# Performance work log

Measured on AMD Instinct MI355X. Metric: run time of the kernel, lower is better.

Reference implementation:

```python
import jax, jax.numpy as jnp
import numpy as np

NUM_CENTROID = 64
HIDDEN = 768
MAX_SEQ = 128
D = MAX_SEQ * HIDDEN  # 98304 flattened feature dim
NUM_ITERS = 10        # fixed Lloyd iterations (original loops to tol; fixed for jit)


def _cdist(x, c):
    x2 = jnp.sum(x * x, axis=-1, keepdims=True)          # [N,1]
    c2 = jnp.sum(c * c, axis=-1)                          # [K]
    d2 = x2 + c2[None, :] - 2.0 * (x @ c.T)               # [N,K]
    return jnp.sqrt(jnp.maximum(d2, 0.0))


def setup_inputs() -> dict:
    key = jax.random.key(0)
    k1, k2 = jax.random.split(key)
    x = jax.random.normal(k1, (1024, MAX_SEQ, HIDDEN), dtype=jnp.float32)
    # centroid table initialized as Normal(mean=0.07, std=0.39) per the module
    centroid = 0.07 + 0.39 * jax.random.normal(k2, (NUM_CENTROID, D), dtype=jnp.float32)
    return {"x": x, "centroid": centroid}


def reference(x, centroid):
    X = x.reshape(-1, D)                                  # [N, D]
    N = X.shape[0]
    # 'resuming' branch: snap each centroid to its nearest sample
    dis0 = _cdist(X, centroid)                            # [N, K]
    choice_points = jnp.argmin(dis0, axis=0)              # [K]
    state = X[choice_points]                              # [K, D]
    ones = jnp.ones((N,), dtype=X.dtype)

    def step(state, _):
        dis = _cdist(X, state)                            # [N, K]
        choice = jnp.argmin(dis, axis=1)                  # [N]
        sums = jax.ops.segment_sum(X, choice, num_segments=NUM_CENTROID)   # [K, D]
        counts = jax.ops.segment_sum(ones, choice, num_segments=NUM_CENTROID)  # [K]
        nonempty = counts[:, None] > 0
        new_state = jnp.where(nonempty, sums / jnp.maximum(counts[:, None], 1.0), state)
        return new_state, choice

    state, choices = jax.lax.scan(step, state, None, length=NUM_ITERS)
    # returns (new centroids, final cluster assignments) like the module
    return state, choices[-1]
```

## Files before the change

### kernel.cpp

```cpp
#include <hip/hip_runtime.h>
#include <cstddef>
#include <cstdint>


#define N_PTS  1024
#define K_C    64
#define D_DIM  98304
#define ITERS  10
#define SPLITD 64
#define BM     64
#define DC     64
#define LDSP   72
#define NCHK   96
#define CCHK   12
#define GSEG   16
#define NPAIR  36
#define GT     128
#define GDC    32
#define GLP    40

typedef __attribute__((ext_vector_type(8))) short bf16x8;
typedef __attribute__((ext_vector_type(8))) unsigned short ushort8;
typedef __attribute__((ext_vector_type(4))) float f32x4;

__device__ __forceinline__ unsigned short f2bf(float x) {
    unsigned u = __float_as_uint(x);
    u = (u + 0x7FFFu + ((u >> 16) & 1u)) >> 16;
    return (unsigned short)u;
}
__device__ __forceinline__ float bf2f(unsigned short b) {
    return __uint_as_float((unsigned)b << 16);
}
__device__ __forceinline__ void cvt2(float x, unsigned short& h, unsigned short& l) {
    h = f2bf(x);
    l = f2bf(x - bf2f(h));
}

__device__ __forceinline__ float block_sum256(float s) {
    #pragma unroll
    for (int o = 32; o; o >>= 1) s += __shfl_down(s, o);
    __shared__ float red[4];
    int lane = threadIdx.x & 63, w = threadIdx.x >> 6;
    if (lane == 0) red[w] = s;
    __syncthreads();
    return red[0] + red[1] + red[2] + red[3];
}

__global__ __launch_bounds__(256) void convert_kernel(const float* __restrict__ A,
                                                      unsigned short* __restrict__ Ph,
                                                      unsigned short* __restrict__ Pl,
                                                      float* __restrict__ sq_part) {
    const int n = blockIdx.x, j = blockIdx.y;
    const size_t base = (size_t)n * D_DIM + (size_t)j * 8192;
    const int t = threadIdx.x;
    float ss = 0.f;
    #pragma unroll
    for (int i = 0; i < 4; ++i) {
        size_t e = base + (size_t)i * 2048 + t * 8;
        float4 a = *reinterpret_cast<const float4*>(A + e);
        float4 b = *reinterpret_cast<const float4*>(A + e + 4);
        ss += a.x*a.x + a.y*a.y + a.z*a.z + a.w*a.w;
        ss += b.x*b.x + b.y*b.y + b.z*b.z + b.w*b.w;
        ushort4 h0, l0, h1, l1;
        cvt2(a.x, h0.x, l0.x); cvt2(a.y, h0.y, l0.y);
        cvt2(a.z, h0.z, l0.z); cvt2(a.w, h0.w, l0.w);
        cvt2(b.x, h1.x, l1.x); cvt2(b.y, h1.y, l1.y);
        cvt2(b.z, h1.z, l1.z); cvt2(b.w, h1.w, l1.w);
        *reinterpret_cast<ushort4*>(Ph + e)     = h0;
        *reinterpret_cast<ushort4*>(Ph + e + 4) = h1;
        *reinterpret_cast<ushort4*>(Pl + e)     = l0;
        *reinterpret_cast<ushort4*>(Pl + e + 4) = l1;
    }
    ss = block_sum256(ss);
    if (t == 0) sq_part[n * CCHK + j] = ss;
}

__global__ __launch_bounds__(256) void reduce_sq_kernel(const float* __restrict__ sq_part,
                                                        float* __restrict__ out, int rows) {
    int n = blockIdx.x * 256 + threadIdx.x;
    if (n >= rows) return;
    float s = 0.f;
    #pragma unroll
    for (int j = 0; j < CCHK; ++j) s += sq_part[n * CCHK + j];
    out[n] = s;
}

__global__ __launch_bounds__(256, 5) void mfma_dot_kernel(const unsigned short* __restrict__ Xh,
                                                          const unsigned short* __restrict__ Xl,
                                                          const unsigned short* __restrict__ Sh,
                                                          const unsigned short* __restrict__ Sl,
                                                          float* __restrict__ partial) {
    __shared__ alignas(16) short Bh[K_C][LDSP];
    __shared__ alignas(16) short Bl[K_C][LDSP];

    const int seg = blockIdx.x, nblk = blockIdx.y;
    const int t = threadIdx.x;
    const int wid = t >> 6, lane = t & 63;
    const int d_begin = seg * (D_DIM / SPLITD);
    const int NCH = (D_DIM / SPLITD) / DC;

    const int arow = nblk * BM + wid * 16 + (lane & 15);
    const int ko = (lane >> 4) * 8;
    const unsigned short* xh = Xh + (size_t)arow * D_DIM;
    const unsigned short* xl = Xl + (size_t)arow * D_DIM;

    const int sr = t >> 2, sc = (t & 3) * 16;
    const unsigned short* shp = Sh + (size_t)sr * D_DIM;
    const unsigned short* slp = Sl + (size_t)sr * D_DIM;

    ushort8 s0, s1, s2, s3;
    bf16x8 aEh0, aEh1, aEl0, aEl1;
    bf16x8 aOh0, aOh1, aOl0, aOl1;

    auto loadB = [&](int d0) {
        s0 = *reinterpret_cast<const ushort8*>(shp + d0 + sc);
        s1 = *reinterpret_cast<const ushort8*>(shp + d0 + sc + 8);
        s2 = *reinterpret_cast<const ushort8*>(slp + d0 + sc);
        s3 = *reinterpret_cast<const ushort8*>(slp + d0 + sc + 8);
    };
    auto storeB = [&]() {
        *reinterpret_cast<ushort8*>(&Bh[sr][sc])     = s0;
        *reinterpret_cast<ushort8*>(&Bh[sr][sc + 8]) = s1;
        *reinterpret_cast<ushort8*>(&Bl[sr][sc])     = s2;
        *reinterpret_cast<ushort8*>(&Bl[sr][sc + 8]) = s3;
    };

    f32x4 acc[4];
    #pragma unroll
    for (int i = 0; i < 4; ++i) acc[i] = f32x4{0.f, 0.f, 0.f, 0.f};

    #define LOADA(bh0, bh1, bl0, bl1, d0)                                        \
        bh0 = *reinterpret_cast<const bf16x8*>(xh + (d0) + ko);                  \
        bh1 = *reinterpret_cast<const bf16x8*>(xh + (d0) + 32 + ko);             \
        bl0 = *reinterpret_cast<const bf16x8*>(xl + (d0) + ko);                  \
        bl1 = *reinterpret_cast<const bf16x8*>(xl + (d0) + 32 + ko);

    #define MFMAS(ah0, ah1, al0, al1)                                            \
        _Pragma("unroll")                                                        \
        for (int nb = 0; nb < 4; ++nb) {                                         \
            const int br = nb * 16 + (lane & 15);                                \
            bf16x8 bh = *reinterpret_cast<const bf16x8*>(&Bh[br][ko]);           \
            bf16x8 bl = *reinterpret_cast<const bf16x8*>(&Bl[br][ko]);           \
            acc[nb] = __builtin_amdgcn_mfma_f32_16x16x32_bf16(ah0, bh, acc[nb], 0, 0, 0); \
            acc[nb] = __builtin_amdgcn_mfma_f32_16x16x32_bf16(ah0, bl, acc[nb], 0, 0, 0); \
            acc[nb] = __builtin_amdgcn_mfma_f32_16x16x32_bf16(al0, bh, acc[nb], 0, 0, 0); \
        }                                                                        \
        _Pragma("unroll")                                                        \
        for (int nb = 0; nb < 4; ++nb) {                                         \
            const int br = nb * 16 + (lane & 15);                                \
            bf16x8 bh = *reinterpret_cast<const bf16x8*>(&Bh[br][32 + ko]);      \
            bf16x8 bl = *reinterpret_cast<const bf16x8*>(&Bl[br][32 + ko]);      \
            acc[nb] = __builtin_amdgcn_mfma_f32_16x16x32_bf16(ah1, bh, acc[nb], 0, 0, 0); \
            acc[nb] = __builtin_amdgcn_mfma_f32_16x16x32_bf16(ah1, bl, acc[nb], 0, 0, 0); \
            acc[nb] = __builtin_amdgcn_mfma_f32_16x16x32_bf16(al1, bh, acc[nb], 0, 0, 0); \
        }

    loadB(d_begin);
    LOADA(aEh0, aEh1, aEl0, aEl1, d_begin);
    for (int c = 0; c < NCH; c += 2) {
        __syncthreads();
        storeB();
        __syncthreads();
        {
            int dn = d_begin + (c + 1) * DC;
            loadB(dn);
            LOADA(aOh0, aOh1, aOl0, aOl1, dn);
        }
        MFMAS(aEh0, aEh1, aEl0, aEl1);
        __syncthreads();
        storeB();
        __syncthreads();
        if (c + 2 < NCH) {
            int dn = d_begin + (c + 2) * DC;
            loadB(dn);
            LOADA(aEh0, aEh1, aEl0, aEl1, dn);
        }
        MFMAS(aOh0, aOh1, aOl0, aOl1);
    }
    #undef LOADA
    #undef MFMAS

    #pragma unroll
    for (int nb = 0; nb < 4; ++nb)
        #pragma unroll
        for (int r = 0; r < 4; ++r) {
            int row = wid * 16 + (lane >> 4) * 4 + r;
            int col = nb * 16 + (lane & 15);
            int n = nblk * BM + row;
            partial[((size_t)seg * N_PTS + n) * K_C + col] = acc[nb][r];
        }
}

__global__ __launch_bounds__(256) void reduce_dot_kernel(const float* __restrict__ partial,
                                                         float* __restrict__ dot) {
    int i = blockIdx.x * 256 + threadIdx.x;
    float s = 0.f;
    #pragma unroll 8
    for (int p = 0; p < SPLITD; ++p) s += partial[(size_t)p * N_PTS * K_C + i];
    dot[i] = s;
}

__global__ __launch_bounds__(256) void argmin_n_kernel(const float* __restrict__ dot,
                                                       const float* __restrict__ x2,
                                                       int* __restrict__ choice_pts) {
    int k = blockIdx.x;
    float best = 3.4e38f; int bi = N_PTS;
    for (int n = threadIdx.x; n < N_PTS; n += 256) {
        float v = fmaf(-2.f, dot[n * K_C + k], x2[n]);
        if (v < best || (v == best && n < bi)) { best = v; bi = n; }
    }
    #pragma unroll
    for (int off = 32; off; off >>= 1) {
        float v2 = __shfl_down(best, off);
        int   i2 = __shfl_down(bi, off);
        if (v2 < best || (v2 == best && i2 < bi)) { best = v2; bi = i2; }
    }
    __shared__ float bv[4]; __shared__ int bix[4];
    int lane = threadIdx.x & 63, wid = threadIdx.x >> 6;
    if (lane == 0) { bv[wid] = best; bix[wid] = bi; }
    __syncthreads();
    if (threadIdx.x == 0) {
        for (int w = 1; w < 4; ++w)
            if (bv[w] < best || (bv[w] == best && bix[w] < bi)) { best = bv[w]; bi = bix[w]; }
        choice_pts[k] = bi;
    }
}

__global__ __launch_bounds__(256) void gather_kernel(const float* __restrict__ X,
                                                     const int* __restrict__ choice_pts,
                                                     float* __restrict__ state) {
    int k = blockIdx.x;
    int c = choice_pts[k];
    size_t d = (size_t)blockIdx.y * 1024 + threadIdx.x * 4;
    float4 v = *reinterpret_cast<const float4*>(X + (size_t)c * D_DIM + d);
    *reinterpret_cast<float4*>(state + (size_t)k * D_DIM + d) = v;
}

__global__ __launch_bounds__(256) void gbuild_kernel(const unsigned short* __restrict__ Xh,
                                                     const unsigned short* __restrict__ Xl,
                                                     float* __restrict__ Gpart) {
    __shared__ alignas(16) short Ah[GT][GLP];
    __shared__ alignas(16) short Al[GT][GLP];
    __shared__ alignas(16) short Bh[GT][GLP];
    __shared__ alignas(16) short Bl[GT][GLP];

    const int p = blockIdx.x, seg = blockIdx.y;
    int bi = 0, rem = p, rl = 8;
    while (rem >= rl) { rem -= rl; --rl; ++bi; }
    const int bj = bi + rem;

    const int t = threadIdx.x;
    const int wid = t >> 6, lane = t & 63;
    const int wr = wid >> 1, wc = wid & 1;
    const int d_begin = seg * (D_DIM / GSEG);
    const int NCH = (D_DIM / GSEG) / GDC;

    const int srow = t >> 1;
    const int scol = (t & 1) << 4;
    const unsigned short* gah = Xh + (size_t)(bi * GT + srow) * D_DIM;
    const unsigned short* gal = Xl + (size_t)(bi * GT + srow) * D_DIM;
    const unsigned short* gbh = Xh + (size_t)(bj * GT + srow) * D_DIM;
    const unsigned short* gbl = Xl + (size_t)(bj * GT + srow) * D_DIM;

    ushort8 ra0, ra1, ra2, ra3, rb0, rb1, rb2, rb3;
    auto loadRegs = [&](int d0) {
        ra0 = *reinterpret_cast<const ushort8*>(gah + d0 + scol);
        ra1 = *reinterpret_cast<const ushort8*>(gah + d0 + scol + 8);
        ra2 = *reinterpret_cast<const ushort8*>(gal + d0 + scol);
        ra3 = *reinterpret_cast<const ushort8*>(gal + d0 + scol + 8);
        rb0 = *reinterpret_cast<const ushort8*>(gbh + d0 + scol);
        rb1 = *reinterpret_cast<const ushort8*>(gbh + d0 + scol + 8);
        rb2 = *reinterpret_cast<const ushort8*>(gbl + d0 + scol);
        rb3 = *reinterpret_cast<const ushort8*>(gbl + d0 + scol + 8);
    };
    auto storeRegs = [&]() {
        *reinterpret_cast<ushort8*>(&Ah[srow][scol])     = ra0;
        *reinterpret_cast<ushort8*>(&Ah[srow][scol + 8]) = ra1;
        *reinterpret_cast<ushort8*>(&Al[srow][scol])     = ra2;
        *reinterpret_cast<ushort8*>(&Al[srow][scol + 8]) = ra3;
        *reinterpret_cast<ushort8*>(&Bh[srow][scol])     = rb0;
        *reinterpret_cast<ushort8*>(&Bh[srow][scol + 8]) = rb1;
        *reinterpret_cast<ushort8*>(&Bl[srow][scol])     = rb2;
        *reinterpret_cast<ushort8*>(&Bl[srow][scol + 8]) = rb3;
    };

    f32x4 acc[4][4];
    #pragma unroll
    for (int i = 0; i < 4; ++i)
        #pragma unroll
        for (int j = 0; j < 4; ++j) acc[i][j] = f32x4{0.f, 0.f, 0.f, 0.f};

    const int rbase = wr * 64 + (lane & 15);
    const int cbase = wc * 64 + (lane & 15);
    const int ko = (lane >> 4) * 8;

    loadRegs(d_begin);
    for (int c = 0; c < NCH; ++c) {
        __syncthreads();
        storeRegs();
        __syncthreads();
        if (c + 1 < NCH) loadRegs(d_begin + (c + 1) * GDC);
        bf16x8 fah[4], fal[4], fbh[4], fbl[4];
        #pragma unroll
        for (int f = 0; f < 4; ++f) {
            fah[f] = *reinterpret_cast<const bf16x8*>(&Ah[rbase + f * 16][ko]);
            fal[f] = *reinterpret_cast<const bf16x8*>(&Al[rbase + f * 16][ko]);
            fbh[f] = *reinterpret_cast<const bf16x8*>(&Bh[cbase + f * 16][ko]);
            fbl[f] = *reinterpret_cast<const bf16x8*>(&Bl[cbase + f * 16][ko]);
        }
        #pragma unroll
        for (int fi = 0; fi < 4; ++fi)
            #pragma unroll
            for (int fj = 0; fj < 4; ++fj) {
                acc[fi][fj] = __builtin_amdgcn_mfma_f32_16x16x32_bf16(fah[fi], fbh[fj], acc[fi][fj], 0, 0, 0);
                acc[fi][fj] = __builtin_amdgcn_mfma_f32_16x16x32_bf16(fah[fi], fbl[fj], acc[fi][fj], 0, 0, 0);
                acc[fi][fj] = __builtin_amdgcn_mfma_f32_16x16x32_bf16(fal[fi], fbh[fj], acc[fi][fj], 0, 0, 0);
            }
    }

    float* gp = Gpart + ((size_t)seg * NPAIR + p) * (GT * GT);
    #pragma unroll
    for (int fi = 0; fi < 4; ++fi)
        #pragma unroll
        for (int fj = 0; fj < 4; ++fj)
            #pragma unroll
            for (int r = 0; r < 4; ++r) {
                int row = wr * 64 + fi * 16 + (lane >> 4) * 4 + r;
                int col = wc * 64 + fj * 16 + (lane & 15);
                gp[row * GT + col] = acc[fi][fj][r];
            }
}

__global__ __launch_bounds__(256) void reduce_g_kernel(const float* __restrict__ Gpart,
                                                       float* __restrict__ G) {
    const int p = blockIdx.x, blk = blockIdx.y;
    int bi = 0, rem = p, rl = 8;
    while (rem >= rl) { rem -= rl; --rl; ++bi; }
    const int bj = bi + rem;
    const int e0 = blk * 1024 + threadIdx.x * 4;
    float sx = 0.f, sy = 0.f, sz = 0.f, sw = 0.f;
    #pragma unroll
    for (int g = 0; g < GSEG; ++g) {
        const float4 v = *reinterpret_cast<const float4*>(
            Gpart + ((size_t)g * NPAIR + p) * (GT * GT) + e0);
        sx += v.x; sy += v.y; sz += v.z; sw += v.w;
    }
    const int row = e0 >> 7, col = e0 & 127;
    const int gi = bi * GT + row, gj = bj * GT + col;
    float4 o = {sx, sy, sz, sw};
    *reinterpret_cast<float4*>(&G[(size_t)gi * N_PTS + gj]) = o;
    if (bi != bj) {
        G[(size_t)(gj + 0) * N_PTS + gi] = sx;
        G[(size_t)(gj + 1) * N_PTS + gi] = sy;
        G[(size_t)(gj + 2) * N_PTS + gi] = sz;
        G[(size_t)(gj + 3) * N_PTS + gi] = sw;
    }
}

__global__ __launch_bounds__(256) void dot0_kernel(const float* __restrict__ G,
                                                   const int* __restrict__ cpts,
                                                   const float* __restrict__ x2,
                                                   float* __restrict__ dot,
                                                   float* __restrict__ c2) {
    int g = blockIdx.x * 256 + threadIdx.x;
    int n = g >> 6, k = g & 63;
    dot[g] = G[(size_t)n * N_PTS + cpts[k]];
    if (g < K_C) c2[g] = x2[cpts[g]];
}

__global__ __launch_bounds__(256) void assign_g_kernel(const float* __restrict__ dot,
                                                       const float* __restrict__ c2,
                                                       int* __restrict__ choice_it) {
    int wid = threadIdx.x >> 6, lane = threadIdx.x & 63;
    int n = blockIdx.x * 4 + wid;
    float v = fmaf(-2.f, dot[n * K_C + lane], c2[lane]);
    int bi = lane;
    #pragma unroll
    for (int m = 32; m; m >>= 1) {
        float v2 = __shfl_xor(v, m);
        int   i2 = __shfl_xor(bi, m);
        if (v2 < v || (v2 == v && i2 < bi)) { v = v2; bi = i2; }
    }
    if (lane == 0) choice_it[n] = bi;
}

__global__ __launch_bounds__(1024) void sort2_kernel(const int* __restrict__ choice,
                                                     int* __restrict__ order,
                                                     int* __restrict__ cstart,
                                                     int* __restrict__ tlast,
                                                     int it) {
    __shared__ int ch[N_PTS];
    __shared__ int cnt[K_C];
    __shared__ int cst[K_C + 1];
    int t = threadIdx.x;
    if (t < K_C) cnt[t] = 0;
    __syncthreads();
    int c = choice[t];
    ch[t] = c;
    atomicAdd(&cnt[c], 1);
    __syncthreads();
    if (t == 0) {
        int a = 0;
        for (int k = 0; k < K_C; ++k) { cst[k] = a; a += cnt[k]; }
        cst[K_C] = a;
    }
    __syncthreads();
    if (t <= K_C) cstart[t] = cst[t];
    if (t < K_C && cnt[t] > 0) tlast[t] = it;
    int r = 0;
    for (int m = 0; m < t; ++m) r += (ch[m] == c);
    order[cst[c] + r] = t;
}

__global__ __launch_bounds__(256) void dotup_kernel(const float* __restrict__ G,
                                                    const int* __restrict__ order,
                                                    const int* __restrict__ cstart,
                                                    float* __restrict__ dot) {
    __shared__ int ord[N_PTS];
    __shared__ int cst[K_C + 1];
    int t = threadIdx.x;
    #pragma unroll
    for (int i = 0; i < 4; ++i) ord[t + 256 * i] = order[t + 256 * i];
    if (t <= K_C) cst[t] = cstart[t];
    __syncthreads();
    int wid = t >> 6, lane = t & 63;
    int n = blockIdx.x * 4 + wid;
    int b = cst[lane], e = cst[lane + 1];
    if (b == e) return;
    const float* gr = G + (size_t)n * N_PTS;
    float s = 0.f;
    for (int i = b; i < e; ++i) s += gr[ord[i]];
    dot[n * K_C + lane] = s / (float)(e - b);
}

__global__ __launch_bounds__(64) void c2up_kernel(const float* __restrict__ dot,
                                                  const int* __restrict__ order,
                                                  const int* __restrict__ cstart,
                                                  float* __restrict__ c2) {
    int k = threadIdx.x;
    int b = cstart[k], e = cstart[k + 1];
    if (b == e) return;
    float s = 0.f;
    for (int i = b; i < e; ++i) s += dot[order[i] * K_C + k];
    c2[k] = s / (float)(e - b);
}

__global__ __launch_bounds__(64) void init_tlast_kernel(int* __restrict__ tlast) {
    tlast[threadIdx.x] = -1;
}

__global__ __launch_bounds__(256) void final_state_kernel(const float* __restrict__ X,
                                                          const int* __restrict__ chbuf,
                                                          const int* __restrict__ tlast,
                                                          float* __restrict__ state) {
    const int k = blockIdx.x;
    const int tk = tlast[k];
    if (tk < 0) return;
    __shared__ int chs[N_PTS];
    const int* src = chbuf + tk * N_PTS;
    const int t = threadIdx.x;
    #pragma unroll
    for (int i = 0; i < 4; ++i) chs[t + 256 * i] = src[t + 256 * i];
    __syncthreads();
    const size_t d = (size_t)blockIdx.y * 1024 + t * 4;
    float sx = 0.f, sy = 0.f, sz = 0.f, sw = 0.f;
    int cm = 0;
    for (int n = 0; n < N_PTS; ++n) {
        if (chs[n] == k) {
            ++cm;
            const float4 v = *reinterpret_cast<const float4*>(X + (size_t)n * D_DIM + d);
            sx += v.x; sy += v.y; sz += v.z; sw += v.w;
        }
    }
    float inv = 1.f / (float)cm;
    float4 o = {sx * inv, sy * inv, sz * inv, sw * inv};
    *reinterpret_cast<float4*>(state + (size_t)k * D_DIM + d) = o;
}

__global__ __launch_bounds__(256) void choice_out_kernel(const int* __restrict__ choice,
                                                         float* __restrict__ out) {
    int n = blockIdx.x * 256 + threadIdx.x;
    if (n < N_PTS) out[n] = (float)choice[n];
}

extern "C" void kernel_launch(void* const* d_in, const int* in_sizes, int n_in,
                              void* d_out, int out_size, void* d_ws, size_t ws_size,
                              hipStream_t stream) {
    const float* X  = (const float*)d_in[0];
    const float* C0 = (const float*)d_in[1];
    float* state      = (float*)d_out;
    float* out_choice = state + (size_t)K_C * D_DIM;

    char* w = (char*)d_ws;
    size_t off = 0;
    auto alloc = [&](size_t bytes) { void* p = w + off; off = (off + bytes + 255) & ~(size_t)255; return p; };
    unsigned short* Xh = (unsigned short*)alloc((size_t)N_PTS * D_DIM * 2);
    unsigned short* Xl = (unsigned short*)alloc((size_t)N_PTS * D_DIM * 2);
    unsigned short* Sh = (unsigned short*)alloc((size_t)K_C * D_DIM * 2);
    unsigned short* Sl = (unsigned short*)alloc((size_t)K_C * D_DIM * 2);
    float* partial = (float*)alloc((size_t)SPLITD * N_PTS * K_C * 4);
    float* Gpart   = (float*)alloc((size_t)GSEG * NPAIR * GT * GT * 4);
    float* G       = (float*)alloc((size_t)N_PTS * N_PTS * 4);
    float* dotb    = (float*)alloc((size_t)N_PTS * K_C * 4);
    float* x2p     = (float*)alloc((size_t)N_PTS * CCHK * 4);
    float* x2      = (float*)alloc((size_t)N_PTS * 4);
    float* c0sq    = (float*)alloc((size_t)K_C * CCHK * 4);
    float* dotg    = (float*)alloc((size_t)N_PTS * K_C * 4);
    float* c2      = (float*)alloc(256);
    int* cpts      = (int*)alloc(256);
    int* chbuf     = (int*)alloc((size_t)ITERS * N_PTS * 4);
    int* order     = (int*)alloc((size_t)N_PTS * 4);
    int* cstart    = (int*)alloc(512);
    int* tlast     = (int*)alloc(256);

    dim3 b256(256);

    convert_kernel<<<dim3(N_PTS, CCHK), b256, 0, stream>>>(X, Xh, Xl, x2p);
    reduce_sq_kernel<<<dim3(4), b256, 0, stream>>>(x2p, x2, N_PTS);

    gbuild_kernel<<<dim3(NPAIR, GSEG), b256, 0, stream>>>(Xh, Xl, Gpart);
    reduce_g_kernel<<<dim3(NPAIR, 16), b256, 0, stream>>>(Gpart, G);

    convert_kernel<<<dim3(K_C, CCHK), b256, 0, stream>>>(C0, Sh, Sl, c0sq);
    mfma_dot_kernel<<<dim3(SPLITD, N_PTS / BM), b256, 0, stream>>>(Xh, Xl, Sh, Sl, partial);
    reduce_dot_kernel<<<dim3(N_PTS * K_C / 256), b256, 0, stream>>>(partial, dotb);
    argmin_n_kernel<<<K_C, b256, 0, stream>>>(dotb, x2, cpts);
    gather_kernel<<<dim3(K_C, NCHK), b256, 0, stream>>>(X, cpts, state);
    init_tlast_kernel<<<1, dim3(64), 0, stream>>>(tlast);
    dot0_kernel<<<dim3(N_PTS * K_C / 256), b256, 0, stream>>>(G, cpts, x2, dotg, c2);

    for (int it = 0; it < ITERS; ++it) {
        assign_g_kernel<<<dim3(N_PTS / 4), b256, 0, stream>>>(dotg, c2, chbuf + it * N_PTS);
        sort2_kernel<<<1, dim3(1024), 0, stream>>>(chbuf + it * N_PTS, order, cstart, tlast, it);
        if (it < ITERS - 1) {
            dotup_kernel<<<dim3(N_PTS / 4), b256, 0, stream>>>(G, order, cstart, dotg);
            c2up_kernel<<<1, dim3(64), 0, stream>>>(dotg, order, cstart, c2);
        }
    }

    final_state_kernel<<<dim3(K_C, NCHK), b256, 0, stream>>>(X, chbuf, tlast, state);
    choice_out_kernel<<<dim3(N_PTS / 256), b256, 0, stream>>>(chbuf + (ITERS - 1) * N_PTS, out_choice);
}
```

Baseline: 2.179 ms.

## Split Gram kernel over more D segments and restructure tile staging

Raises the number of D-dimension segments in the Gram-matrix kernel from 16 to 96, so far more blocks run (36 pairs x 96) and each does a shorter reduction. Global-to-LDS staging now has four threads per row, each loading one 8-element granule for two row halves, and the LDS row padding is removed. The cost is six times more partial-sum traffic written to and read back by the reduce kernel, whose loop unroll is cut to 8. Dropping the padding may also add LDS bank conflicts on the fragment reads.

```diff
diff --git a/kernel.cpp b/kernel.cpp
--- a/kernel.cpp
+++ b/kernel.cpp
@@ -13,11 +13,11 @@
 #define LDSP   72
 #define NCHK   96
 #define CCHK   12
-#define GSEG   16
+#define GSEG   96
 #define NPAIR  36
 #define GT     128
 #define GDC    32
-#define GLP    40
+#define GLP    32
 
 typedef __attribute__((ext_vector_type(8))) short bf16x8;
 typedef __attribute__((ext_vector_type(8))) unsigned short ushort8;
@@ -255,33 +255,37 @@
     const int d_begin = seg * (D_DIM / GSEG);
     const int NCH = (D_DIM / GSEG) / GDC;
 
-    const int srow = t >> 1;
-    const int scol = (t & 1) << 4;
-    const unsigned short* gah = Xh + (size_t)(bi * GT + srow) * D_DIM;
-    const unsigned short* gal = Xl + (size_t)(bi * GT + srow) * D_DIM;
-    const unsigned short* gbh = Xh + (size_t)(bj * GT + srow) * D_DIM;
-    const unsigned short* gbl = Xl + (size_t)(bj * GT + srow) * D_DIM;
-
-    ushort8 ra0, ra1, ra2, ra3, rb0, rb1, rb2, rb3;
+    const int strow = t >> 2;
+    const int sgran = (t & 3) * 8;
+    const unsigned short* a0h = Xh + (size_t)(bi * GT + strow) * D_DIM;
+    const unsigned short* a1h = Xh + (size_t)(bi * GT + 64 + strow) * D_DIM;
+    const unsigned short* a0l = Xl + (size_t)(bi * GT + strow) * D_DIM;
+    const unsigned short* a1l = Xl + (size_t)(bi * GT + 64 + strow) * D_DIM;
+    const unsigned short* b0h = Xh + (size_t)(bj * GT + strow) * D_DIM;
+    const unsigned short* b1h = Xh + (size_t)(bj * GT + 64 + strow) * D_DIM;
+    const unsigned short* b0l = Xl + (size_t)(bj * GT + strow) * D_DIM;
+    const unsigned short* b1l = Xl + (size_t)(bj * GT + 64 + strow) * D_DIM;
+
+    ushort8 rA0h, rA1h, rA0l, rA1l, rB0h, rB1h, rB0l, rB1l;
     auto loadRegs = [&](int d0) {
-        ra0 = *reinterpret_cast<const ushort8*>(gah + d0 + scol);
-        ra1 = *reinterpret_cast<const ushort8*>(gah + d0 + scol + 8);
-        ra2 = *reinterpret_cast<const ushort8*>(gal + d0 + scol);
-        ra3 = *reinterpret_cast<const ushort8*>(gal + d0 + scol + 8);
-        rb0 = *reinterpret_cast<const ushort8*>(gbh + d0 + scol);
-        rb1 = *reinterpret_cast<const ushort8*>(gbh + d0 + scol + 8);
-        rb2 = *reinterpret_cast<const ushort8*>(gbl + d0 + scol);
-        rb3 = *reinterpret_cast<const ushort8*>(gbl + d0 + scol + 8);
+        rA0h = *reinterpret_cast<const ushort8*>(a0h + d0 + sgran);
+        rA1h = *reinterpret_cast<const ushort8*>(a1h + d0 + sgran);
+        rA0l = *reinterpret_cast<const ushort8*>(a0l + d0 + sgran);
+        rA1l = *reinterpret_cast<const ushort8*>(a1l + d0 + sgran);
+        rB0h = *reinterpret_cast<const ushort8*>(b0h + d0 + sgran);
+        rB1h = *reinterpret_cast<const ushort8*>(b1h + d0 + sgran);
+        rB0l = *reinterpret_cast<const ushort8*>(b0l + d0 + sgran);
+        rB1l = *reinterpret_cast<const ushort8*>(b1l + d0 + sgran);
     };
     auto storeRegs = [&]() {
-        *reinterpret_cast<ushort8*>(&Ah[srow][scol])     = ra0;
-        *reinterpret_cast<ushort8*>(&Ah[srow][scol + 8]) = ra1;
-        *reinterpret_cast<ushort8*>(&Al[srow][scol])     = ra2;
-        *reinterpret_cast<ushort8*>(&Al[srow][scol + 8]) = ra3;
-        *reinterpret_cast<ushort8*>(&Bh[srow][scol])     = rb0;
-        *reinterpret_cast<ushort8*>(&Bh[srow][scol + 8]) = rb1;
-        *reinterpret_cast<ushort8*>(&Bl[srow][scol])     = rb2;
-        *reinterpret_cast<ushort8*>(&Bl[srow][scol + 8]) = rb3;
+        *reinterpret_cast<ushort8*>(&Ah[strow][sgran])      = rA0h;
+        *reinterpret_cast<ushort8*>(&Ah[64 + strow][sgran]) = rA1h;
+        *reinterpret_cast<ushort8*>(&Al[strow][sgran])      = rA0l;
+        *reinterpret_cast<ushort8*>(&Al[64 + strow][sgran]) = rA1l;
+        *reinterpret_cast<ushort8*>(&Bh[strow][sgran])      = rB0h;
+        *reinterpret_cast<ushort8*>(&Bh[64 + strow][sgran]) = rB1h;
+        *reinterpret_cast<ushort8*>(&Bl[strow][sgran])      = rB0l;
+        *reinterpret_cast<ushort8*>(&Bl[64 + strow][sgran]) = rB1l;
     };
 
     f32x4 acc[4][4];
@@ -339,7 +343,7 @@
     const int bj = bi + rem;
     const int e0 = blk * 1024 + threadIdx.x * 4;
     float sx = 0.f, sy = 0.f, sz = 0.f, sw = 0.f;
-    #pragma unroll
+    #pragma unroll 8
     for (int g = 0; g < GSEG; ++g) {
         const float4 v = *reinterpret_cast<const float4*>(
             Gpart + ((size_t)g * NPAIR + p) * (GT * GT) + e0);
```

New measurement: 2.230 ms. 2.4% more time.

## Restructure Gram build: A operands direct to registers, interleaved D shards, grouped block order

Applied to the files above, without the earlier changes.

The Gram-matrix kernel now loads the A-side fragments straight from global memory into registers, double-buffered in even/odd sets, and stages only the B tile through LDS. This halves the LDS footprint and removes the A stores and reads from LDS. The D dimension is split into interleaved 512-wide shards instead of contiguous segments. Blocks are launched in a 1D order that groups eight shards of the same pair together, which should improve L2 locality across concurrent blocks. The mfma_dot_kernel occupancy hint is also dropped, and the A-side global loads are uncoalesced 16-byte per-lane reads, which may cost memory efficiency.

```diff
diff --git a/kernel.cpp b/kernel.cpp
--- a/kernel.cpp
+++ b/kernel.cpp
@@ -13,11 +13,13 @@
 #define LDSP   72
 #define NCHK   96
 #define CCHK   12
-#define GSEG   16
+#define NGRP   16
+#define SHPG   12
+#define SHW    512
 #define NPAIR  36
 #define GT     128
 #define GDC    32
-#define GLP    40
+#define GLP    32
 
 typedef __attribute__((ext_vector_type(8))) short bf16x8;
 typedef __attribute__((ext_vector_type(8))) unsigned short ushort8;
@@ -85,11 +87,11 @@
     out[n] = s;
 }
 
-__global__ __launch_bounds__(256, 5) void mfma_dot_kernel(const unsigned short* __restrict__ Xh,
-                                                          const unsigned short* __restrict__ Xl,
-                                                          const unsigned short* __restrict__ Sh,
-                                                          const unsigned short* __restrict__ Sl,
-                                                          float* __restrict__ partial) {
+__global__ __launch_bounds__(256) void mfma_dot_kernel(const unsigned short* __restrict__ Xh,
+                                                       const unsigned short* __restrict__ Xl,
+                                                       const unsigned short* __restrict__ Sh,
+                                                       const unsigned short* __restrict__ Sl,
+                                                       float* __restrict__ partial) {
     __shared__ alignas(16) short Bh[K_C][LDSP];
     __shared__ alignas(16) short Bl[K_C][LDSP];
 
@@ -239,12 +241,13 @@
 __global__ __launch_bounds__(256) void gbuild_kernel(const unsigned short* __restrict__ Xh,
                                                      const unsigned short* __restrict__ Xl,
                                                      float* __restrict__ Gpart) {
-    __shared__ alignas(16) short Ah[GT][GLP];
-    __shared__ alignas(16) short Al[GT][GLP];
     __shared__ alignas(16) short Bh[GT][GLP];
     __shared__ alignas(16) short Bl[GT][GLP];
 
-    const int p = blockIdx.x, seg = blockIdx.y;
+    const int id = blockIdx.x;
+    const int r = id & 7, q = id >> 3;
+    const int p = q % NPAIR;
+    const int g = ((q / NPAIR) << 3) + r;
     int bi = 0, rem = p, rl = 8;
     while (rem >= rl) { rem -= rl; --rl; ++bi; }
     const int bj = bi + rem;
@@ -252,36 +255,32 @@
     const int t = threadIdx.x;
     const int wid = t >> 6, lane = t & 63;
     const int wr = wid >> 1, wc = wid & 1;
-    const int d_begin = seg * (D_DIM / GSEG);
-    const int NCH = (D_DIM / GSEG) / GDC;
-
-    const int srow = t >> 1;
-    const int scol = (t & 1) << 4;
-    const unsigned short* gah = Xh + (size_t)(bi * GT + srow) * D_DIM;
-    const unsigned short* gal = Xl + (size_t)(bi * GT + srow) * D_DIM;
-    const unsigned short* gbh = Xh + (size_t)(bj * GT + srow) * D_DIM;
-    const unsigned short* gbl = Xl + (size_t)(bj * GT + srow) * D_DIM;
-
-    ushort8 ra0, ra1, ra2, ra3, rb0, rb1, rb2, rb3;
-    auto loadRegs = [&](int d0) {
-        ra0 = *reinterpret_cast<const ushort8*>(gah + d0 + scol);
-        ra1 = *reinterpret_cast<const ushort8*>(gah + d0 + scol + 8);
-        ra2 = *reinterpret_cast<const ushort8*>(gal + d0 + scol);
-        ra3 = *reinterpret_cast<const ushort8*>(gal + d0 + scol + 8);
-        rb0 = *reinterpret_cast<const ushort8*>(gbh + d0 + scol);
-        rb1 = *reinterpret_cast<const ushort8*>(gbh + d0 + scol + 8);
-        rb2 = *reinterpret_cast<const ushort8*>(gbl + d0 + scol);
-        rb3 = *reinterpret_cast<const ushort8*>(gbl + d0 + scol + 8);
+    const int ko = (lane >> 4) * 8;
+
+    const int arow = bi * GT + wr * 64 + (lane & 15);
+    const unsigned short* xhA = Xh + (size_t)arow * D_DIM + ko;
+    const unsigned short* xlA = Xl + (size_t)arow * D_DIM + ko;
+
+    const int strow = t >> 2, sgran = (t & 3) * 8;
+    const unsigned short* b0h = Xh + (size_t)(bj * GT + strow) * D_DIM + sgran;
+    const unsigned short* b1h = Xh + (size_t)(bj * GT + 64 + strow) * D_DIM + sgran;
+    const unsigned short* b0l = Xl + (size_t)(bj * GT + strow) * D_DIM + sgran;
+    const unsigned short* b1l = Xl + (size_t)(bj * GT + 64 + strow) * D_DIM + sgran;
+
+    ushort8 sB0h, sB1h, sB0l, sB1l;
+    bf16x8 ahE[4], alE[4], ahO[4], alO[4];
+
+    auto loadB = [&](int d0) {
+        sB0h = *reinterpret_cast<const ushort8*>(b0h + d0);
+        sB1h = *reinterpret_cast<const ushort8*>(b1h + d0);
+        sB0l = *reinterpret_cast<const ushort8*>(b0l + d0);
+        sB1l = *reinterpret_cast<const ushort8*>(b1l + d0);
     };
-    auto storeRegs = [&]() {
-        *reinterpret_cast<ushort8*>(&Ah[srow][scol])     = ra0;
-        *reinterpret_cast<ushort8*>(&Ah[srow][scol + 8]) = ra1;
-        *reinterpret_cast<ushort8*>(&Al[srow][scol])     = ra2;
-        *reinterpret_cast<ushort8*>(&Al[srow][scol + 8]) = ra3;
-        *reinterpret_cast<ushort8*>(&Bh[srow][scol])     = rb0;
-        *reinterpret_cast<ushort8*>(&Bh[srow][scol + 8]) = rb1;
-        *reinterpret_cast<ushort8*>(&Bl[srow][scol])     = rb2;
-        *reinterpret_cast<ushort8*>(&Bl[srow][scol + 8]) = rb3;
+    auto storeB = [&]() {
+        *reinterpret_cast<ushort8*>(&Bh[strow][sgran])      = sB0h;
+        *reinterpret_cast<ushort8*>(&Bh[64 + strow][sgran]) = sB1h;
+        *reinterpret_cast<ushort8*>(&Bl[strow][sgran])      = sB0l;
+        *reinterpret_cast<ushort8*>(&Bl[64 + strow][sgran]) = sB1l;
     };
 
     f32x4 acc[4][4];
@@ -290,44 +289,71 @@
         #pragma unroll
         for (int j = 0; j < 4; ++j) acc[i][j] = f32x4{0.f, 0.f, 0.f, 0.f};
 
-    const int rbase = wr * 64 + (lane & 15);
     const int cbase = wc * 64 + (lane & 15);
-    const int ko = (lane >> 4) * 8;
-
-    loadRegs(d_begin);
-    for (int c = 0; c < NCH; ++c) {
-        __syncthreads();
-        storeRegs();
-        __syncthreads();
-        if (c + 1 < NCH) loadRegs(d_begin + (c + 1) * GDC);
-        bf16x8 fah[4], fal[4], fbh[4], fbl[4];
-        #pragma unroll
-        for (int f = 0; f < 4; ++f) {
-            fah[f] = *reinterpret_cast<const bf16x8*>(&Ah[rbase + f * 16][ko]);
-            fal[f] = *reinterpret_cast<const bf16x8*>(&Al[rbase + f * 16][ko]);
-            fbh[f] = *reinterpret_cast<const bf16x8*>(&Bh[cbase + f * 16][ko]);
-            fbl[f] = *reinterpret_cast<const bf16x8*>(&Bl[cbase + f * 16][ko]);
-        }
-        #pragma unroll
-        for (int fi = 0; fi < 4; ++fi)
-            #pragma unroll
-            for (int fj = 0; fj < 4; ++fj) {
-                acc[fi][fj] = __builtin_amdgcn_mfma_f32_16x16x32_bf16(fah[fi], fbh[fj], acc[fi][fj], 0, 0, 0);
-                acc[fi][fj] = __builtin_amdgcn_mfma_f32_16x16x32_bf16(fah[fi], fbl[fj], acc[fi][fj], 0, 0, 0);
-                acc[fi][fj] = __builtin_amdgcn_mfma_f32_16x16x32_bf16(fal[fi], fbh[fj], acc[fi][fj], 0, 0, 0);
-            }
-    }
-
-    float* gp = Gpart + ((size_t)seg * NPAIR + p) * (GT * GT);
+    const int NCHT = SHPG * (SHW / GDC);
+    #define D0_OF(idx) ((g + (((idx) >> 4) << 4)) * SHW + ((idx) & 15) * GDC)
+
+    #define LOADA(ah, al, d0)                                                   \
+        _Pragma("unroll")                                                       \
+        for (int fi = 0; fi < 4; ++fi) {                                        \
+            ah[fi] = *reinterpret_cast<const bf16x8*>(xhA + (size_t)fi * 16 * D_DIM + (d0)); \
+            al[fi] = *reinterpret_cast<const bf16x8*>(xlA + (size_t)fi * 16 * D_DIM + (d0)); \
+        }
+
+    #define MFMAS(ah, al)                                                       \
+        {                                                                       \
+            bf16x8 fbh[4], fbl[4];                                              \
+            _Pragma("unroll")                                                   \
+            for (int fj = 0; fj < 4; ++fj) {                                    \
+                fbh[fj] = *reinterpret_cast<const bf16x8*>(&Bh[cbase + fj * 16][ko]); \
+                fbl[fj] = *reinterpret_cast<const bf16x8*>(&Bl[cbase + fj * 16][ko]); \
+            }                                                                   \
+            _Pragma("unroll")                                                   \
+            for (int fi = 0; fi < 4; ++fi)                                      \
+                _Pragma("unroll")                                               \
+                for (int fj = 0; fj < 4; ++fj) {                                \
+                    acc[fi][fj] = __builtin_amdgcn_mfma_f32_16x16x32_bf16(ah[fi], fbh[fj], acc[fi][fj], 0, 0, 0); \
+                    acc[fi][fj] = __builtin_amdgcn_mfma_f32_16x16x32_bf16(ah[fi], fbl[fj], acc[fi][fj], 0, 0, 0); \
+                    acc[fi][fj] = __builtin_amdgcn_mfma_f32_16x16x32_bf16(al[fi], fbh[fj], acc[fi][fj], 0, 0, 0); \
+                }                                                               \
+        }
+
+    loadB(D0_OF(0));
+    LOADA(ahE, alE, D0_OF(0));
+    for (int idx = 0; idx < NCHT; idx += 2) {
+        __syncthreads();
+        storeB();
+        __syncthreads();
+        {
+            int dn = D0_OF(idx + 1);
+            loadB(dn);
+            LOADA(ahO, alO, dn);
+        }
+        MFMAS(ahE, alE);
+        __syncthreads();
+        storeB();
+        __syncthreads();
+        if (idx + 2 < NCHT) {
+            int dn = D0_OF(idx + 2);
+            loadB(dn);
+            LOADA(ahE, alE, dn);
+        }
+        MFMAS(ahO, alO);
+    }
+    #undef D0_OF
+    #undef LOADA
+    #undef MFMAS
+
+    float* gp = Gpart + ((size_t)g * NPAIR + p) * (GT * GT);
     #pragma unroll
     for (int fi = 0; fi < 4; ++fi)
         #pragma unroll
         for (int fj = 0; fj < 4; ++fj)
             #pragma unroll
-            for (int r = 0; r < 4; ++r) {
-                int row = wr * 64 + fi * 16 + (lane >> 4) * 4 + r;
+            for (int r2 = 0; r2 < 4; ++r2) {
+                int row = wr * 64 + fi * 16 + (lane >> 4) * 4 + r2;
                 int col = wc * 64 + fj * 16 + (lane & 15);
-                gp[row * GT + col] = acc[fi][fj][r];
+                gp[row * GT + col] = acc[fi][fj][r2];
             }
 }
 
@@ -340,7 +366,7 @@
     const int e0 = blk * 1024 + threadIdx.x * 4;
     float sx = 0.f, sy = 0.f, sz = 0.f, sw = 0.f;
     #pragma unroll
-    for (int g = 0; g < GSEG; ++g) {
+    for (int g = 0; g < NGRP; ++g) {
         const float4 v = *reinterpret_cast<const float4*>(
             Gpart + ((size_t)g * NPAIR + p) * (GT * GT) + e0);
         sx += v.x; sy += v.y; sz += v.z; sw += v.w;
@@ -499,7 +525,7 @@
     unsigned short* Sh = (unsigned short*)alloc((size_t)K_C * D_DIM * 2);
     unsigned short* Sl = (unsigned short*)alloc((size_t)K_C * D_DIM * 2);
     float* partial = (float*)alloc((size_t)SPLITD * N_PTS * K_C * 4);
-    float* Gpart   = (float*)alloc((size_t)GSEG * NPAIR * GT * GT * 4);
+    float* Gpart   = (float*)alloc((size_t)NGRP * NPAIR * GT * GT * 4);
     float* G       = (float*)alloc((size_t)N_PTS * N_PTS * 4);
     float* dotb    = (float*)alloc((size_t)N_PTS * K_C * 4);
     float* x2p     = (float*)alloc((size_t)N_PTS * CCHK * 4);
@@ -518,7 +544,7 @@
     convert_kernel<<<dim3(N_PTS, CCHK), b256, 0, stream>>>(X, Xh, Xl, x2p);
     reduce_sq_kernel<<<dim3(4), b256, 0, stream>>>(x2p, x2, N_PTS);
 
-    gbuild_kernel<<<dim3(NPAIR, GSEG), b256, 0, stream>>>(Xh, Xl, Gpart);
+    gbuild_kernel<<<dim3(8 * NPAIR * (NGRP / 8)), b256, 0, stream>>>(Xh, Xl, Gpart);
     reduce_g_kernel<<<dim3(NPAIR, 16), b256, 0, stream>>>(Gpart, G);
 
     convert_kernel<<<dim3(K_C, CCHK), b256, 0, stream>>>(C0, Sh, Sl, c0sq);
```

Measured after the change: 2.263 ms. 3.9% more time.

## Rewrite Gram build with direct global-to-LDS loads, swizzled tiles, and finer D split

Applied to the files above, without the earlier changes.

The Gram-matrix kernel now stages tiles with global_load_lds (direct DMA into LDS) into an XOR-swizzled layout instead of loading through registers and storing to padded LDS. The D dimension is split into 32 interleaved groups instead of 16 contiguous segments, and the block index is remapped so neighbouring blocks work on different groups. The goal is higher occupancy and more parallelism, with less register pressure and fewer LDS bank conflicts. In exchange the register prefetch overlap is lost, since each chunk now waits at a barrier, and the partial-sum buffer and its reduction double in size.

```diff
diff --git a/kernel.cpp b/kernel.cpp
--- a/kernel.cpp
+++ b/kernel.cpp
@@ -13,11 +13,13 @@
 #define LDSP   72
 #define NCHK   96
 #define CCHK   12
-#define GSEG   16
+#define NGRP   32
+#define SHPG   6
+#define SHW    512
+#define NCHT   96
 #define NPAIR  36
 #define GT     128
 #define GDC    32
-#define GLP    40
 
 typedef __attribute__((ext_vector_type(8))) short bf16x8;
 typedef __attribute__((ext_vector_type(8))) unsigned short ushort8;
@@ -34,6 +36,12 @@
 __device__ __forceinline__ void cvt2(float x, unsigned short& h, unsigned short& l) {
     h = f2bf(x);
     l = f2bf(x - bf2f(h));
+}
+
+__device__ __forceinline__ void gload_lds16(const unsigned short* g, char* l) {
+    __builtin_amdgcn_global_load_lds(
+        (const __attribute__((address_space(1))) unsigned int*)g,
+        (__attribute__((address_space(3))) unsigned int*)l, 16, 0, 0);
 }
 
 __device__ __forceinline__ float block_sum256(float s) {
@@ -85,11 +93,11 @@
     out[n] = s;
 }
 
-__global__ __launch_bounds__(256, 5) void mfma_dot_kernel(const unsigned short* __restrict__ Xh,
-                                                          const unsigned short* __restrict__ Xl,
-                                                          const unsigned short* __restrict__ Sh,
-                                                          const unsigned short* __restrict__ Sl,
-                                                          float* __restrict__ partial) {
+__global__ __launch_bounds__(256) void mfma_dot_kernel(const unsigned short* __restrict__ Xh,
+                                                       const unsigned short* __restrict__ Xl,
+                                                       const unsigned short* __restrict__ Sh,
+                                                       const unsigned short* __restrict__ Sl,
+                                                       float* __restrict__ partial) {
     __shared__ alignas(16) short Bh[K_C][LDSP];
     __shared__ alignas(16) short Bl[K_C][LDSP];
 
@@ -236,15 +244,16 @@
     *reinterpret_cast<float4*>(state + (size_t)k * D_DIM + d) = v;
 }
 
-__global__ __launch_bounds__(256) void gbuild_kernel(const unsigned short* __restrict__ Xh,
-                                                     const unsigned short* __restrict__ Xl,
-                                                     float* __restrict__ Gpart) {
-    __shared__ alignas(16) short Ah[GT][GLP];
-    __shared__ alignas(16) short Al[GT][GLP];
-    __shared__ alignas(16) short Bh[GT][GLP];
-    __shared__ alignas(16) short Bl[GT][GLP];
-
-    const int p = blockIdx.x, seg = blockIdx.y;
+__global__ __launch_bounds__(256, 3) void gbuild_kernel(const unsigned short* __restrict__ Xh,
+                                                        const unsigned short* __restrict__ Xl,
+                                                        float* __restrict__ Gpart) {
+    __shared__ alignas(16) char LA[16384];
+    __shared__ alignas(16) char LB[16384];
+
+    const int id = blockIdx.x;
+    const int xr = id & 7, q = id >> 3;
+    const int p = q % NPAIR;
+    const int g = ((q / NPAIR) << 3) + xr;
     int bi = 0, rem = p, rl = 8;
     while (rem >= rl) { rem -= rl; --rl; ++bi; }
     const int bj = bi + rem;
@@ -252,37 +261,22 @@
     const int t = threadIdx.x;
     const int wid = t >> 6, lane = t & 63;
     const int wr = wid >> 1, wc = wid & 1;
-    const int d_begin = seg * (D_DIM / GSEG);
-    const int NCH = (D_DIM / GSEG) / GDC;
-
-    const int srow = t >> 1;
-    const int scol = (t & 1) << 4;
-    const unsigned short* gah = Xh + (size_t)(bi * GT + srow) * D_DIM;
-    const unsigned short* gal = Xl + (size_t)(bi * GT + srow) * D_DIM;
-    const unsigned short* gbh = Xh + (size_t)(bj * GT + srow) * D_DIM;
-    const unsigned short* gbl = Xl + (size_t)(bj * GT + srow) * D_DIM;
-
-    ushort8 ra0, ra1, ra2, ra3, rb0, rb1, rb2, rb3;
-    auto loadRegs = [&](int d0) {
-        ra0 = *reinterpret_cast<const ushort8*>(gah + d0 + scol);
-        ra1 = *reinterpret_cast<const ushort8*>(gah + d0 + scol + 8);
-        ra2 = *reinterpret_cast<const ushort8*>(gal + d0 + scol);
-        ra3 = *reinterpret_cast<const ushort8*>(gal + d0 + scol + 8);
-        rb0 = *reinterpret_cast<const ushort8*>(gbh + d0 + scol);
-        rb1 = *reinterpret_cast<const ushort8*>(gbh + d0 + scol + 8);
-        rb2 = *reinterpret_cast<const ushort8*>(gbl + d0 + scol);
-        rb3 = *reinterpret_cast<const ushort8*>(gbl + d0 + scol + 8);
-    };
-    auto storeRegs = [&]() {
-        *reinterpret_cast<ushort8*>(&Ah[srow][scol])     = ra0;
-        *reinterpret_cast<ushort8*>(&Ah[srow][scol + 8]) = ra1;
-        *reinterpret_cast<ushort8*>(&Al[srow][scol])     = ra2;
-        *reinterpret_cast<ushort8*>(&Al[srow][scol + 8]) = ra3;
-        *reinterpret_cast<ushort8*>(&Bh[srow][scol])     = rb0;
-        *reinterpret_cast<ushort8*>(&Bh[srow][scol + 8]) = rb1;
-        *reinterpret_cast<ushort8*>(&Bl[srow][scol])     = rb2;
-        *reinterpret_cast<ushort8*>(&Bl[srow][scol + 8]) = rb3;
-    };
+
+    const int isA = (wid < 2) ? 1 : 0;
+    const int i0 = (wid & 1) * 8;
+    char* ltile = isA ? LA : LB;
+    const int rowbase = (isA ? bi : bj) * GT;
+    const int lw = (lane & 7) ^ (lane >> 3);
+    const unsigned short* plane = (lw & 4) ? Xl : Xh;
+    const unsigned short* gbase[8];
+    #pragma unroll
+    for (int j = 0; j < 8; ++j)
+        gbase[j] = plane + (size_t)(rowbase + (i0 + j) * 8 + (lane >> 3)) * D_DIM + (lw & 3) * 8;
+
+    const int sh = (lane >> 4) ^ (lane & 7);
+    const int sl = (4 + (lane >> 4)) ^ (lane & 7);
+    const int ra0 = (wr * 64 + (lane & 15)) * 128;
+    const int rb0 = (wc * 64 + (lane & 15)) * 128;
 
     f32x4 acc[4][4];
     #pragma unroll
@@ -290,44 +284,42 @@
         #pragma unroll
         for (int j = 0; j < 4; ++j) acc[i][j] = f32x4{0.f, 0.f, 0.f, 0.f};
 
-    const int rbase = wr * 64 + (lane & 15);
-    const int cbase = wc * 64 + (lane & 15);
-    const int ko = (lane >> 4) * 8;
-
-    loadRegs(d_begin);
-    for (int c = 0; c < NCH; ++c) {
+    for (int idx = 0; idx < NCHT; ++idx) {
+        const int d0 = (g + ((idx >> 4) << 5)) * SHW + (idx & 15) * GDC;
         __syncthreads();
-        storeRegs();
+        #pragma unroll
+        for (int j = 0; j < 8; ++j)
+            gload_lds16(gbase[j] + d0, ltile + (i0 + j) * 1024);
         __syncthreads();
-        if (c + 1 < NCH) loadRegs(d_begin + (c + 1) * GDC);
-        bf16x8 fah[4], fal[4], fbh[4], fbl[4];
+        bf16x8 ah[4], al[4];
         #pragma unroll
-        for (int f = 0; f < 4; ++f) {
-            fah[f] = *reinterpret_cast<const bf16x8*>(&Ah[rbase + f * 16][ko]);
-            fal[f] = *reinterpret_cast<const bf16x8*>(&Al[rbase + f * 16][ko]);
-            fbh[f] = *reinterpret_cast<const bf16x8*>(&Bh[cbase + f * 16][ko]);
-            fbl[f] = *reinterpret_cast<const bf16x8*>(&Bl[cbase + f * 16][ko]);
+        for (int fi = 0; fi < 4; ++fi) {
+            ah[fi] = *reinterpret_cast<const bf16x8*>(LA + ra0 + fi * 2048 + sh * 16);
+            al[fi] = *reinterpret_cast<const bf16x8*>(LA + ra0 + fi * 2048 + sl * 16);
         }
         #pragma unroll
-        for (int fi = 0; fi < 4; ++fi)
+        for (int fj = 0; fj < 4; ++fj) {
+            bf16x8 bh = *reinterpret_cast<const bf16x8*>(LB + rb0 + fj * 2048 + sh * 16);
+            bf16x8 bl = *reinterpret_cast<const bf16x8*>(LB + rb0 + fj * 2048 + sl * 16);
             #pragma unroll
-            for (int fj = 0; fj < 4; ++fj) {
-                acc[fi][fj] = __builtin_amdgcn_mfma_f32_16x16x32_bf16(fah[fi], fbh[fj], acc[fi][fj], 0, 0, 0);
-                acc[fi][fj] = __builtin_amdgcn_mfma_f32_16x16x32_bf16(fah[fi], fbl[fj], acc[fi][fj], 0, 0, 0);
-                acc[fi][fj] = __builtin_amdgcn_mfma_f32_16x16x32_bf16(fal[fi], fbh[fj], acc[fi][fj], 0, 0, 0);
+            for (int fi = 0; fi < 4; ++fi) {
+                acc[fi][fj] = __builtin_amdgcn_mfma_f32_16x16x32_bf16(ah[fi], bh, acc[fi][fj], 0, 0, 0);
+                acc[fi][fj] = __builtin_amdgcn_mfma_f32_16x16x32_bf16(ah[fi], bl, acc[fi][fj], 0, 0, 0);
+                acc[fi][fj] = __builtin_amdgcn_mfma_f32_16x16x32_bf16(al[fi], bh, acc[fi][fj], 0, 0, 0);
             }
-    }
-
-    float* gp = Gpart + ((size_t)seg * NPAIR + p) * (GT * GT);
+        }
+    }
+
+    float* gp = Gpart + ((size_t)g * NPAIR + p) * (GT * GT);
     #pragma unroll
     for (int fi = 0; fi < 4; ++fi)
         #pragma unroll
         for (int fj = 0; fj < 4; ++fj)
             #pragma unroll
-            for (int r = 0; r < 4; ++r) {
-                int row = wr * 64 + fi * 16 + (lane >> 4) * 4 + r;
+            for (int r2 = 0; r2 < 4; ++r2) {
+                int row = wr * 64 + fi * 16 + (lane >> 4) * 4 + r2;
                 int col = wc * 64 + fj * 16 + (lane & 15);
-                gp[row * GT + col] = acc[fi][fj][r];
+                gp[row * GT + col] = acc[fi][fj][r2];
             }
 }
 
@@ -339,8 +331,8 @@
     const int bj = bi + rem;
     const int e0 = blk * 1024 + threadIdx.x * 4;
     float sx = 0.f, sy = 0.f, sz = 0.f, sw = 0.f;
-    #pragma unroll
-    for (int g = 0; g < GSEG; ++g) {
+    #pragma unroll 8
+    for (int g = 0; g < NGRP; ++g) {
         const float4 v = *reinterpret_cast<const float4*>(
             Gpart + ((size_t)g * NPAIR + p) * (GT * GT) + e0);
         sx += v.x; sy += v.y; sz += v.z; sw += v.w;
@@ -499,7 +491,7 @@
     unsigned short* Sh = (unsigned short*)alloc((size_t)K_C * D_DIM * 2);
     unsigned short* Sl = (unsigned short*)alloc((size_t)K_C * D_DIM * 2);
     float* partial = (float*)alloc((size_t)SPLITD * N_PTS * K_C * 4);
-    float* Gpart   = (float*)alloc((size_t)GSEG * NPAIR * GT * GT * 4);
+    float* Gpart   = (float*)alloc((size_t)NGRP * NPAIR * GT * GT * 4);
     float* G       = (float*)alloc((size_t)N_PTS * N_PTS * 4);
     float* dotb    = (float*)alloc((size_t)N_PTS * K_C * 4);
     float* x2p     = (float*)alloc((size_t)N_PTS * CCHK * 4);
@@ -518,7 +510,7 @@
     convert_kernel<<<dim3(N_PTS, CCHK), b256, 0, stream>>>(X, Xh, Xl, x2p);
     reduce_sq_kernel<<<dim3(4), b256, 0, stream>>>(x2p, x2, N_PTS);
 
-    gbuild_kernel<<<dim3(NPAIR, GSEG), b256, 0, stream>>>(Xh, Xl, Gpart);
+    gbuild_kernel<<<dim3(8 * NPAIR * (NGRP / 8)), b256, 0, stream>>>(Xh, Xl, Gpart);
     reduce_g_kernel<<<dim3(NPAIR, 16), b256, 0, stream>>>(Gpart, G);
 
     convert_kernel<<<dim3(K_C, CCHK), b256, 0, stream>>>(C0, Sh, Sl, c0sq);
```

Result: faster. 1.928 ms (-11.5%).
